# Kernel tuning notes

Measured on AMD Instinct MI355X. Metric: run time of the kernel, lower is better.

## Reference

```python
import jax, jax.numpy as jnp
from jax import lax
import numpy as np

B, T, DIN, DMID, DOUT = 8, 512, 512, 512, 128
KER = (0.15, 0.7, 0.15)  # 3-tap Gaussian blur, midnum fixed at 0.7 (deterministic stand-in for random.uniform(0.55,0.9))


def setup_inputs() -> dict:
    key = jax.random.key(0)
    ks = jax.random.split(key, 14)
    def lin(k, fi, fo):
        s = (6.0 / (fi + fo)) ** 0.5  # xavier-uniform
        return jax.random.uniform(k, (fi, fo), jnp.float32, -s, s)
    def convw(k, co, ci, kh, kw):
        s = (6.0 / (ci * kh * kw + co * kh * kw)) ** 0.5
        return jax.random.uniform(k, (co, ci, kh, kw), jnp.float32, -s, s)
    return {
        "seq": jax.random.normal(ks[0], (B, T, DIN), jnp.float32),
        "len_seq": jax.random.randint(ks[1], (B,), 256, T + 1, jnp.int32),
        "W1": lin(ks[2], DIN, DMID), "b1": jnp.zeros((DMID,), jnp.float32),
        "W2": lin(ks[3], DMID, DMID), "b2": jnp.zeros((DMID,), jnp.float32),
        "W3": lin(ks[4], DMID, DOUT), "b3": jnp.zeros((DOUT,), jnp.float32),
        "c1w": convw(ks[5], 30, 2, 5, 5), "c1b": jnp.zeros((30,), jnp.float32),
        "c2w": convw(ks[6], 30, 30, 5, 5), "c2b": jnp.zeros((30,), jnp.float32),
        "c3w": convw(ks[7], 1, 30, 3, 3), "c3b": jnp.zeros((1,), jnp.float32),
    }


def _mlp(x, W1, b1, W2, b2, W3, b3):
    # SequenceInception: linear-relu-linear-relu-linear, then L2 normalize with nan/inf -> 0
    h = jax.nn.relu(x @ W1 + b1)
    h = jax.nn.relu(h @ W2 + b2)
    o = h @ W3 + b3
    n = jnp.linalg.norm(o, axis=-1, keepdims=True)
    return jnp.nan_to_num(o / n, nan=0.0, posinf=0.0, neginf=0.0)


def _conv(x, w, b, pad):
    y = lax.conv_general_dilated(x, w, (1, 1), ((pad, pad), (pad, pad)),
                                 dimension_numbers=("NCHW", "OIHW", "NCHW"))
    return y + b[None, :, None, None]


def _blur(seq, len_seq):
    # BlurGenerationPair (Tc>4, 3-tap kernel, stride 1 branch), fully batched.
    k0, k1, k2 = KER
    blur = k0 * seq[:, :-2] + k1 * seq[:, 1:-1] + k2 * seq[:, 2:]  # [B, T-2, D]
    blur = jnp.pad(blur, ((0, 0), (0, 2), (0, 0)))
    t = jnp.arange(T)
    out_len = len_seq - 2
    out_mask = (t[None, :] < out_len[:, None]).astype(seq.dtype)      # [B, T]
    avged_seq = blur * out_mask[:, :, None]
    R = jnp.where(t[None] < len_seq[:, None], (t + 1.0) / len_seq[:, None].astype(jnp.float32), 0.0)
    avged_R = jnp.where(t[None] < out_len[:, None], (t + 1.0) / out_len[:, None].astype(jnp.float32), 0.0)
    # SeqtoBlur[b, i+o, i] = ker[o] for column i < out_len[b]
    base = k0 * jnp.eye(T) + k1 * jnp.eye(T, k=-1) + k2 * jnp.eye(T, k=-2)  # [T(row), T(col)]
    SeqtoBlur = base[None, :, :] * out_mask[:, None, :]
    sg = lax.stop_gradient
    return sg(SeqtoBlur), sg(avged_seq), sg(R), sg(avged_R), out_len


def reference(seq, len_seq, W1, b1, W2, b2, W3, b3, c1w, c1b, c2w, c2b, c3w, c3b):
    SeqtoBlur, avged_seq, R, avged_R, avged_len = _blur(seq, len_seq)
    emb_q = _mlp(seq, W1, b1, W2, b2, W3, b3)        # [B, T, DOUT]
    emb_k = _mlp(avged_seq, W1, b1, W2, b2, W3, b3)  # [B, T, DOUT]
    # OPA, batched over B (original asserts batch==1 and loops; same math per sample)
    sq = jnp.sum(emb_q * emb_q, -1)
    sk = jnp.sum(emb_k * emb_k, -1)
    g = jnp.einsum("bqd,bkd->bqk", emb_q, emb_k)
    D = jnp.sqrt(jnp.clip(sq[:, :, None] + sk[:, None, :] - 2.0 * g, 1e-12))  # cdist p=2
    P = jnp.abs(R[:, :, None] - avged_R[:, None, :])                           # 1-D cdist
    A = jnp.stack([D, P], axis=1)                    # [B, 2, T, T]
    A = jax.nn.relu(_conv(A, c1w, c1b, 2))
    A = jax.nn.relu(_conv(A, c2w, c2b, 2))
    A = _conv(A, c3w, c3b, 1)[:, 0] + D              # [B, T, T]
    S = jax.nn.softmax(-A, axis=2)
    At = S / jnp.sum(jnp.abs(S), axis=(1, 2), keepdims=True)  # L1 normalize over T*T
    dis = jnp.sum(D * At, axis=(1, 2))               # [B]
    return S, dis, SeqtoBlur, avged_len
```

## Files before the change

kernel.cpp:

```cpp
#include <hip/hip_runtime.h>
#include <hip/hip_bf16.h>

static constexpr size_t CHW = (size_t)512*512*32;

static constexpr size_t S_OFF    = 0;
static constexpr size_t DIS_OFF  = (size_t)8*512*512;
static constexpr size_t S2B_OFF  = DIS_OFF + 8;
static constexpr size_t ALEN_OFF = S2B_OFF + (size_t)8*512*512;

typedef __attribute__((ext_vector_type(8))) short bf16x8;
typedef __attribute__((ext_vector_type(4))) float f32x4;

__device__ __forceinline__ unsigned short rne_bf16(float x) {
  unsigned u = __builtin_bit_cast(unsigned, x);
  return (unsigned short)((u + 0x7FFFu + ((u >> 16) & 1u)) >> 16);
}
__device__ __forceinline__ unsigned pack_bf16x2(float lo, float hi) {
  return (unsigned)rne_bf16(lo) | ((unsigned)rne_bf16(hi) << 16);
}
__device__ __forceinline__ float bf2f(short s) {
  return __builtin_bit_cast(float, ((unsigned)(unsigned short)s) << 16);
}
__device__ __forceinline__ int chlog(int p) { return (p & 1) ? 16 + (p >> 1) : (p >> 1); }

__global__ __launch_bounds__(128) void megaprep(
    const float* __restrict__ seq, const int* __restrict__ len,
    const float* __restrict__ W1, const float* __restrict__ W2, const float* __restrict__ W3,
    const float* __restrict__ c1w, const float* __restrict__ c2w, const float* __restrict__ c3w,
    unsigned short* __restrict__ QKb,
    unsigned short* __restrict__ W1T, unsigned short* __restrict__ W2T,
    unsigned short* __restrict__ W3T,
    unsigned short* __restrict__ WB1m, unsigned char* __restrict__ WB2f,
    float* __restrict__ WT3, float* __restrict__ zpage,
    float* __restrict__ R, float* __restrict__ AR, float* __restrict__ alenOut,
    float* __restrict__ s2b) {
  int bid = blockIdx.x, tid = threadIdx.x;
  if (bid < 8192) {
    int t = bid & 511, b = (bid >> 9) & 7, mode = bid >> 12;
    size_t base = ((size_t)b*512 + t)*512 + tid*4;
    float v[4] = {0.f, 0.f, 0.f, 0.f};
    if (mode == 0) {
      float4 a = *(const float4*)&seq[base];
      v[0]=a.x; v[1]=a.y; v[2]=a.z; v[3]=a.w;
    } else {
      int OL = len[b] - 2;
      if (t < OL) {
        float4 a = *(const float4*)&seq[base];
        float4 c = *(const float4*)&seq[base + 512];
        float4 d = *(const float4*)&seq[base + 1024];
        v[0] = 0.15f*a.x + 0.7f*c.x + 0.15f*d.x;
        v[1] = 0.15f*a.y + 0.7f*c.y + 0.15f*d.y;
        v[2] = 0.15f*a.z + 0.7f*c.z + 0.15f*d.z;
        v[3] = 0.15f*a.w + 0.7f*c.w + 0.15f*d.w;
      }
    }
    ushort4 h;
    h.x = rne_bf16(v[0]); h.y = rne_bf16(v[1]);
    h.z = rne_bf16(v[2]); h.w = rne_bf16(v[3]);
    *(ushort4*)&QKb[((size_t)(mode*4096 + b*512 + t))*512 + tid*4] = h;
    return;
  }
  if (bid < 12288) {
    int r = bid - 8192;
    int i = r & 511, b = r >> 9;
    int OL = len[b] - 2;
    int j0 = tid*4;
    float vals[4];
#pragma unroll
    for (int e = 0; e < 4; ++e) {
      int j = j0 + e;
      float x = 0.f;
      if (j < OL) {
        if (j == i)        x = 0.15f;
        else if (j == i-1) x = 0.7f;
        else if (j == i-2) x = 0.15f;
      }
      vals[e] = x;
    }
    *(float4*)&s2b[((size_t)b*512 + i)*512 + j0] =
        make_float4(vals[0],vals[1],vals[2],vals[3]);
    return;
  }
  if (bid < 12320) {
    int r = bid - 12288;
    int b = r >> 2, t = (r & 3)*128 + tid;
    int L = len[b], OL = L - 2;
    R[b*512+t]  = (t < L)  ? (t+1.f)/(float)L  : 0.f;
    AR[b*512+t] = (t < OL) ? (t+1.f)/(float)OL : 0.f;
    if (t == 0) alenOut[b] = (float)OL;
    return;
  }
  if (bid < 13472) {
    int n = bid - 12320;
    const float* W; unsigned short* WT; int col, N;
    if (n < 512)       { W = W1; WT = W1T; col = n;        N = 512; }
    else if (n < 1024) { W = W2; WT = W2T; col = n - 512;  N = 512; }
    else               { W = W3; WT = W3T; col = n - 1024; N = 128; }
    for (int k = tid; k < 512; k += 128)
      WT[(size_t)col*512 + k] = rne_bf16(W[(size_t)k*N + col]);
    return;
  }
  if (tid < 64) zpage[tid] = 0.f;
  for (int i = tid; i < 7168; i += 128) {
    int ts = i >> 8, r = i & 255, oc = r >> 3, ch = r & 7;
    float v = 0.f;
    if (ts < 25 && oc < 30 && ch < 2) v = c1w[oc*50 + ch*25 + ts];
    WB1m[i] = rne_bf16(v);
  }
  for (int i = tid; i < 12800; i += 128) {
    int tap = i >> 9, r = i & 511, oc = r >> 4, jj = r & 15;
    float v0 = (oc < 30 && jj < 30)      ? c2w[(size_t)(oc*30 + jj)*25 + tap]      : 0.f;
    float v1 = (oc < 30 && 16 + jj < 30) ? c2w[(size_t)(oc*30 + 16 + jj)*25 + tap] : 0.f;
    int pk = __builtin_amdgcn_cvt_pk_fp8_f32(v0, v1, 0, false);
    ((unsigned short*)WB2f)[(tap*32 + oc)*16 + jj] = (unsigned short)pk;
  }
  for (int i = tid; i < 288; i += 128) {
    int tap = i >> 5, icp = i & 31;
    int icl = chlog(icp);
    WT3[i] = (icl < 30) ? c3w[icl*9 + tap] : 0.f;
  }
}

template<int OUTMODE>
__global__ __launch_bounds__(256) void gemm_bf(
    const unsigned short* __restrict__ A, const unsigned short* __restrict__ B,
    const float* __restrict__ bias, float* __restrict__ Cf,
    unsigned short* __restrict__ Cb, int M, int N, int K) {
  __shared__ short sA[128*40], sB[64*40];
  int tid = threadIdx.x, l = tid & 63, w = tid >> 6;
  int wm = w >> 1, wn = w & 1;
  int rowBase = blockIdx.y * 128, colBase = blockIdx.x * 64;
  int lr = l & 15, lc = l >> 4;
  f32x4 acc[4][2] = {};
  for (int k0 = 0; k0 < K; k0 += 32) {
    int idx = tid;
#pragma unroll
    for (int it = 0; it < 2; ++it, idx += 256) {
      int row = idx >> 2, c = (idx & 3) * 8;
      *(bf16x8*)&sA[row*40 + c] = *(const bf16x8*)&A[(size_t)(rowBase + row)*K + k0 + c];
    }
    {
      int row = tid >> 2, c = (tid & 3) * 8;
      if (row < 64)
        *(bf16x8*)&sB[row*40 + c] = *(const bf16x8*)&B[(size_t)(colBase + row)*K + k0 + c];
    }
    __syncthreads();
    bf16x8 a[4], b[2];
#pragma unroll
    for (int m = 0; m < 4; ++m)
      a[m] = *(const bf16x8*)&sA[(wm*64 + m*16 + lr)*40 + lc*8];
#pragma unroll
    for (int n = 0; n < 2; ++n)
      b[n] = *(const bf16x8*)&sB[(wn*32 + n*16 + lr)*40 + lc*8];
#pragma unroll
    for (int m = 0; m < 4; ++m)
#pragma unroll
      for (int n = 0; n < 2; ++n)
        acc[m][n] = __builtin_amdgcn_mfma_f32_16x16x32_bf16(a[m], b[n], acc[m][n], 0, 0, 0);
    __syncthreads();
  }
#pragma unroll
  for (int m = 0; m < 4; ++m) {
    int row = rowBase + wm*64 + m*16 + lc*4;
#pragma unroll
    for (int n = 0; n < 2; ++n) {
      int col = colBase + wn*32 + n*16 + lr;
      float bv = bias[col];
#pragma unroll
      for (int j = 0; j < 4; ++j) {
        float v = acc[m][n][j] + bv;
        size_t o = (size_t)(row + j) * N + col;
        if (OUTMODE == 1) Cb[o] = rne_bf16(fmaxf(v, 0.f));
        else              Cf[o] = v;
      }
    }
  }
}

__global__ __launch_bounds__(64) void norm_kernel(const float* __restrict__ EMB,
    unsigned short* __restrict__ Eb, float* __restrict__ sqn) {
  int row = blockIdx.x, tid = threadIdx.x;
  size_t base = (size_t)row * 128;
  float v0 = EMB[base + tid], v1 = EMB[base + tid + 64];
  float ss = v0*v0 + v1*v1;
#pragma unroll
  for (int off = 32; off; off >>= 1) ss += __shfl_xor(ss, off);
  float n = sqrtf(ss);
  float inv = (n > 0.f) ? 1.f/n : 0.f;
  Eb[base + tid]      = rne_bf16(v0 * inv);
  Eb[base + tid + 64] = rne_bf16(v1 * inv);
  if (tid == 0) sqn[row] = ss * inv * inv;
}

__global__ __launch_bounds__(256) void dmat_mfma(const unsigned short* __restrict__ Eb,
    const float* __restrict__ sqn, float* __restrict__ Dm) {
  __shared__ short sQ[64*40], sK[64*40];
  int tid = threadIdx.x, l = tid & 63, w = tid >> 6;
  int wm = w >> 1, wn = w & 1;
  int kBase = blockIdx.x * 64, qBase = blockIdx.y * 64, b = blockIdx.z;
  const unsigned short* Q  = Eb + (size_t)b*512*128;
  const unsigned short* Kp = Eb + (size_t)(4096 + b*512)*128;
  int lr = l & 15, lc = l >> 4;
  f32x4 acc[2][2] = {};
  for (int k0 = 0; k0 < 128; k0 += 32) {
    int row = tid >> 2, c = (tid & 3) * 8;
    *(bf16x8*)&sQ[row*40 + c] = *(const bf16x8*)&Q[(size_t)(qBase + row)*128 + k0 + c];
    *(bf16x8*)&sK[row*40 + c] = *(const bf16x8*)&Kp[(size_t)(kBase + row)*128 + k0 + c];
    __syncthreads();
    bf16x8 q[2], k[2];
#pragma unroll
    for (int m = 0; m < 2; ++m) q[m] = *(const bf16x8*)&sQ[(wm*32 + m*16 + lr)*40 + lc*8];
#pragma unroll
    for (int n = 0; n < 2; ++n) k[n] = *(const bf16x8*)&sK[(wn*32 + n*16 + lr)*40 + lc*8];
#pragma unroll
    for (int m = 0; m < 2; ++m)
#pragma unroll
      for (int n = 0; n < 2; ++n)
        acc[m][n] = __builtin_amdgcn_mfma_f32_16x16x32_bf16(q[m], k[n], acc[m][n], 0, 0, 0);
    __syncthreads();
  }
#pragma unroll
  for (int m = 0; m < 2; ++m) {
#pragma unroll
    for (int n = 0; n < 2; ++n) {
      int k = kBase + wn*32 + n*16 + lr;
      float skv = sqn[4096 + b*512 + k];
#pragma unroll
      for (int j = 0; j < 4; ++j) {
        int q = qBase + wm*32 + m*16 + lc*4 + j;
        float sqv = sqn[b*512 + q];
        float d2 = fmaxf(sqv + skv - 2.f*acc[m][n][j], 1e-12f);
        Dm[((size_t)b*512 + q)*512 + k] = sqrtf(d2);
      }
    }
  }
}

__global__ __launch_bounds__(256) void conv1_mfma(const float* __restrict__ Dm,
    const float* __restrict__ R, const float* __restrict__ AR,
    unsigned char* __restrict__ cbout, const unsigned short* __restrict__ WB1m,
    const float* __restrict__ bias, int b0) {
  __shared__ short tile[36*20*8];
  int tid = threadIdx.x, l = tid & 63, w = tid >> 6;
  int x0 = blockIdx.x * 16, y0 = blockIdx.y * 32, slot = blockIdx.z;
  int b = b0 + slot;
  for (int i = tid; i < 720; i += 256) {
    int r = i / 20, c = i - r*20;
    int gy = y0 - 2 + r, gx = x0 - 2 + c;
    float dv = 0.f, pv = 0.f;
    if ((unsigned)gy < 512u && (unsigned)gx < 512u) {
      dv = Dm[((size_t)b*512 + gy)*512 + gx];
      pv = fabsf(R[b*512 + gy] - AR[b*512 + gx]);
    }
    bf16x8 v = {};
    v[0] = (short)rne_bf16(dv);
    v[1] = (short)rne_bf16(pv);
    *(bf16x8*)&tile[i*8] = v;
  }
  __syncthreads();
  int lr = l & 15, lc = l >> 4;
  f32x4 acc[8][2] = {};
  int wy = w * 8;
  bf16x8 pb0 = *(const bf16x8*)&WB1m[(size_t)lc*256 + lr*8];
  bf16x8 pb1 = *(const bf16x8*)&WB1m[(size_t)lc*256 + (16 + lr)*8];
  __builtin_amdgcn_s_setprio(1);
#pragma unroll
  for (int m = 0; m < 7; ++m) {
    int t = m*4 + lc;
    int ky = t / 5, kx = t - ky*5;
    bool valid = (t < 25);
    bf16x8 b0 = pb0, b1 = pb1;
    if (m < 6) {
      int tn = (m+1)*4 + lc;
      pb0 = *(const bf16x8*)&WB1m[(size_t)tn*256 + lr*8];
      pb1 = *(const bf16x8*)&WB1m[(size_t)tn*256 + (16 + lr)*8];
    }
#pragma unroll
    for (int g = 0; g < 8; ++g) {
      bf16x8 a = {};
      if (valid) a = *(const bf16x8*)&tile[((wy + g + ky)*20 + lr + kx)*8];
      acc[g][0] = __builtin_amdgcn_mfma_f32_16x16x32_bf16(a, b0, acc[g][0], 0, 0, 0);
      acc[g][1] = __builtin_amdgcn_mfma_f32_16x16x32_bf16(a, b1, acc[g][1], 0, 0, 0);
    }
  }
  __builtin_amdgcn_s_setprio(0);
  unsigned char* outp = cbout + (size_t)slot * CHW;
  float bv0 = bias[lr];
  float bv1 = (16 + lr < 30) ? bias[16 + lr] : 0.f;
#pragma unroll
  for (int g = 0; g < 8; ++g) {
    int y = y0 + wy + g;
#pragma unroll
    for (int j = 0; j < 4; ++j) {
      int px = x0 + lc*4 + j;
      size_t ob = ((size_t)y*512 + px)*32;
      int pk = __builtin_amdgcn_cvt_pk_fp8_f32(
          fmaxf(acc[g][0][j] + bv0, 0.f), fmaxf(acc[g][1][j] + bv1, 0.f), 0, false);
      *(unsigned short*)&outp[ob + 2*lr] = (unsigned short)pk;
    }
  }
}

__global__ __launch_bounds__(256, 4) void conv2_mfma(const unsigned char* __restrict__ cbin,
    unsigned short* __restrict__ cbout, const unsigned char* __restrict__ WB2f,
    const float* __restrict__ bias, const float* __restrict__ zpage) {
  __shared__ char tile[36*20*32];
  int tid = threadIdx.x, l = tid & 63, w = tid >> 6;
  int x0 = blockIdx.x * 16, y0 = blockIdx.y * 32, slot = blockIdx.z;
  const unsigned char* in = cbin + (size_t)slot * CHW;
  for (int idx = tid; idx < 1440; idx += 256) {
    int cs = idx & 1, px = idx >> 1;
    int r = px / 20, cc = px - r*20;
    int c16 = cs ^ ((cc >> 1) & 1);
    int gy = y0 - 2 + r, gx = x0 - 2 + cc;
    const void* src = ((unsigned)gy < 512u && (unsigned)gx < 512u)
        ? (const void*)&in[((size_t)gy*512 + gx)*32 + c16*16]
        : (const void*)zpage;
    __builtin_amdgcn_global_load_lds(
        (const __attribute__((address_space(1))) void*)src,
        (__attribute__((address_space(3))) void*)&tile[(size_t)idx*16], 16, 0, 0);
  }
  __syncthreads();
  int lr = l & 15, lc = l >> 4;
  f32x4 acc[8][2] = {};
  int wy = w * 8;
  long long pb0[2], pb1[2];
  {
    pb0[0] = *(const long long*)&WB2f[(size_t)(0*32 + lr)*32 + lc*8];
    pb1[0] = *(const long long*)&WB2f[(size_t)(0*32 + 16 + lr)*32 + lc*8];
    pb0[1] = *(const long long*)&WB2f[(size_t)(5*32 + lr)*32 + lc*8];
    pb1[1] = *(const long long*)&WB2f[(size_t)(5*32 + 16 + lr)*32 + lc*8];
  }
  __builtin_amdgcn_s_setprio(1);
#pragma unroll
  for (int kx = 0; kx < 5; ++kx) {
    int x = lr + kx;
    int s = (((lc >> 1) ^ ((x >> 1) & 1)) << 1) | (lc & 1);
    long long a[12];
#pragma unroll
    for (int r = 0; r < 12; ++r)
      a[r] = *(const long long*)&tile[((wy + r)*20 + x)*32 + s*8];
#pragma unroll
    for (int ky = 0; ky < 5; ++ky) {
      int i = kx*5 + ky;
      int sq = i & 1;
      long long b0 = pb0[sq], b1 = pb1[sq];
      int in2 = i + 2;
      if (in2 < 25) {
        int nkx = in2 / 5, nky = in2 - nkx*5;
        int ntap = nky*5 + nkx;
        pb0[sq] = *(const long long*)&WB2f[(size_t)(ntap*32 + lr)*32 + lc*8];
        pb1[sq] = *(const long long*)&WB2f[(size_t)(ntap*32 + 16 + lr)*32 + lc*8];
      }
#pragma unroll
      for (int g = 0; g < 8; ++g) {
        acc[g][0] = __builtin_amdgcn_mfma_f32_16x16x32_fp8_fp8(a[g+ky], b0, acc[g][0], 0, 0, 0);
        acc[g][1] = __builtin_amdgcn_mfma_f32_16x16x32_fp8_fp8(a[g+ky], b1, acc[g][1], 0, 0, 0);
      }
    }
  }
  __builtin_amdgcn_s_setprio(0);
  unsigned short* outp = cbout + (size_t)slot * CHW;
  float bv0 = (lr < 30) ? bias[lr] : 0.f;
  float bv1 = 0.f;
  if (16 + lr < 30) bv1 = bias[16 + lr];
#pragma unroll
  for (int g = 0; g < 8; ++g) {
    int y = y0 + wy + g;
#pragma unroll
    for (int j = 0; j < 4; ++j) {
      int px = x0 + lc*4 + j;
      size_t ob = ((size_t)y*512 + px)*32;
      *(unsigned*)&outp[ob + 2*lr] =
          pack_bf16x2(fmaxf(acc[g][0][j] + bv0, 0.f), fmaxf(acc[g][1][j] + bv1, 0.f));
    }
  }
}

__global__ __launch_bounds__(256) void conv3_nhwc(const unsigned short* __restrict__ cbin,
    const float* __restrict__ Dm, const float* __restrict__ WT3,
    const float* __restrict__ b3c, float* __restrict__ A3, int b0) {
  int slot = blockIdx.z, b = b0 + slot;
  int tid = threadIdx.x, tx = tid & 15, ty = tid >> 4;
  int x0 = blockIdx.x * 16, y0 = blockIdx.y * 16;
  __shared__ short tile[18*18*40];
  const unsigned short* in = cbin + (size_t)slot * CHW;
  for (int idx = tid; idx < 1296; idx += 256) {
    int c = (idx & 3) * 8, px = idx >> 2;
    int r = px / 18, cc = px - r*18;
    int gy = y0 - 1 + r, gx = x0 - 1 + cc;
    bf16x8 v = {};
    if ((unsigned)gy < 512u && (unsigned)gx < 512u)
      v = *(const bf16x8*)&in[((size_t)gy*512 + gx)*32 + c];
    *(bf16x8*)&tile[(r*18 + cc)*40 + c] = v;
  }
  __syncthreads();
  float acc = 0.f;
#pragma unroll
  for (int ky = 0; ky < 3; ++ky) {
#pragma unroll
    for (int kx = 0; kx < 3; ++kx) {
      const float* wp = &WT3[(ky*3 + kx)*32];
      int base = ((ty+ky)*18 + tx+kx)*40;
#pragma unroll
      for (int c = 0; c < 4; ++c) {
        bf16x8 v = *(const bf16x8*)&tile[base + c*8];
#pragma unroll
        for (int j = 0; j < 8; ++j)
          acc = fmaf(bf2f(v[j]), wp[c*8 + j], acc);
      }
    }
  }
  size_t o = ((size_t)b*512 + y0 + ty)*512 + x0 + tx;
  A3[o] = acc + b3c[0] + Dm[o];
}

__global__ __launch_bounds__(256) void softmax_kernel(const float* __restrict__ A3,
    const float* __restrict__ Dm, float* __restrict__ S,
    float* __restrict__ rowDS, float* __restrict__ rowSS) {
  __shared__ float sred[4];
  __shared__ float sred2[4], sred3[4];
  int q = blockIdx.x, b = blockIdx.y, tid = threadIdx.x;
  size_t base = ((size_t)b*512 + q)*512;
  float x0 = -A3[base + tid], x1 = -A3[base + tid + 256];
  float m = fmaxf(x0, x1);
#pragma unroll
  for (int off = 32; off; off >>= 1) m = fmaxf(m, __shfl_xor(m, off));
  if ((tid & 63) == 0) sred[tid >> 6] = m;
  __syncthreads();
  m = fmaxf(fmaxf(sred[0], sred[1]), fmaxf(sred[2], sred[3]));
  __syncthreads();
  float p0 = expf(x0 - m), p1 = expf(x1 - m);
  float s = p0 + p1;
#pragma unroll
  for (int off = 32; off; off >>= 1) s += __shfl_xor(s, off);
  if ((tid & 63) == 0) sred[tid >> 6] = s;
  __syncthreads();
  s = sred[0] + sred[1] + sred[2] + sred[3];
  float inv = 1.f / s;
  float s0 = p0 * inv, s1 = p1 * inv;
  S[base + tid] = s0;
  S[base + tid + 256] = s1;
  float ds = s0*Dm[base + tid] + s1*Dm[base + tid + 256];
  float ssum = s0 + s1;
#pragma unroll
  for (int off = 32; off; off >>= 1) { ds += __shfl_xor(ds, off); ssum += __shfl_xor(ssum, off); }
  if ((tid & 63) == 0) { sred2[tid>>6] = ds; sred3[tid>>6] = ssum; }
  __syncthreads();
  if (tid == 0) {
    rowDS[b*512+q] = sred2[0]+sred2[1]+sred2[2]+sred2[3];
    rowSS[b*512+q] = sred3[0]+sred3[1]+sred3[2]+sred3[3];
  }
}

__global__ __launch_bounds__(512) void dis_kernel(const float* __restrict__ rowDS,
    const float* __restrict__ rowSS, float* __restrict__ disOut) {
  __shared__ float sd[8], se[8];
  int b = blockIdx.x, tid = threadIdx.x;
  float ds = rowDS[b*512 + tid];
  float ss = rowSS[b*512 + tid];
#pragma unroll
  for (int off = 32; off; off >>= 1) { ds += __shfl_xor(ds, off); ss += __shfl_xor(ss, off); }
  if ((tid & 63) == 0) { sd[tid>>6] = ds; se[tid>>6] = ss; }
  __syncthreads();
  if (tid == 0) {
    float a = 0.f, c = 0.f;
    for (int i = 0; i < 8; ++i) { a += sd[i]; c += se[i]; }
    disOut[b] = a / c;
  }
}

extern "C" void kernel_launch(void* const* d_in, const int* in_sizes, int n_in,
                              void* d_out, int out_size, void* d_ws, size_t ws_size,
                              hipStream_t stream) {
  const float* seq = (const float*)d_in[0];
  const int*   len = (const int*)d_in[1];
  const float* W1  = (const float*)d_in[2];  const float* b1 = (const float*)d_in[3];
  const float* W2  = (const float*)d_in[4];  const float* b2 = (const float*)d_in[5];
  const float* W3  = (const float*)d_in[6];  const float* b3 = (const float*)d_in[7];
  const float* c1w = (const float*)d_in[8];  const float* c1b = (const float*)d_in[9];
  const float* c2w = (const float*)d_in[10]; const float* c2b = (const float*)d_in[11];
  const float* c3w = (const float*)d_in[12]; const float* c3b = (const float*)d_in[13];
  float* out = (float*)d_out;
  char*  ws  = (char*)d_ws;

  size_t off = 0;
  auto alloc = [&](size_t bytes) { size_t o = off; off = (off + bytes + 255) & ~(size_t)255; return o; };
  const size_t MK2 = (size_t)8192*512*2;
  unsigned short* QKb = (unsigned short*)(ws + alloc(MK2));
  unsigned short* H1  = (unsigned short*)(ws + alloc(MK2));
  unsigned short* H2  = (unsigned short*)(ws + alloc(MK2));
  float* EMB = (float*)(ws + alloc((size_t)8192*128*4));
  unsigned short* EMBb = (unsigned short*)(ws + alloc((size_t)8192*128*2));
  float* SQN = (float*)(ws + alloc(8192*4));
  float* Rb  = (float*)(ws + alloc(4096*4));
  float* ARb = (float*)(ws + alloc(4096*4));
  float* Db  = (float*)(ws + alloc((size_t)8*512*512*4));
  float* A3  = (float*)(ws + alloc((size_t)8*512*512*4));
  float* RDS = (float*)(ws + alloc(4096*4));
  float* RSS = (float*)(ws + alloc(4096*4));
  unsigned short* W1T = (unsigned short*)(ws + alloc((size_t)512*512*2));
  unsigned short* W2T = (unsigned short*)(ws + alloc((size_t)512*512*2));
  unsigned short* W3T = (unsigned short*)(ws + alloc((size_t)128*512*2));
  unsigned short* WB1m = (unsigned short*)(ws + alloc(7168*2));
  unsigned char* WB2f = (unsigned char*)(ws + alloc(25600));
  float* WT3 = (float*)(ws + alloc(288*4));
  float* ZPG = (float*)(ws + alloc(256));
  size_t fixed = off;

  int nb = 1;
  const size_t CB1B = CHW;
  const size_t CB2B = CHW * 2;
  if      (fixed + 8*(CB1B + CB2B) <= ws_size) nb = 8;
  else if (fixed + 4*(CB1B + CB2B) <= ws_size) nb = 4;
  else if (fixed + 2*(CB1B + CB2B) <= ws_size) nb = 2;
  unsigned char*  CB1 = (unsigned char*)(ws + alloc((size_t)nb*CB1B));
  unsigned short* CB2 = (unsigned short*)(ws + alloc((size_t)nb*CB2B));

  megaprep<<<13473, 128, 0, stream>>>(seq, len, W1, W2, W3, c1w, c2w, c3w,
      QKb, W1T, W2T, W3T, WB1m, WB2f, WT3, ZPG, Rb, ARb, out + ALEN_OFF, out + S2B_OFF);

  gemm_bf<1><<<dim3(8, 64), 256, 0, stream>>>(QKb, W1T, b1, nullptr, H1, 8192, 512, 512);
  gemm_bf<1><<<dim3(8, 64), 256, 0, stream>>>(H1,  W2T, b2, nullptr, H2, 8192, 512, 512);
  gemm_bf<0><<<dim3(2, 64), 256, 0, stream>>>(H2,  W3T, b3, EMB, nullptr, 8192, 128, 512);
  norm_kernel<<<8192, 64, 0, stream>>>(EMB, EMBb, SQN);
  dmat_mfma<<<dim3(8,8,8), 256, 0, stream>>>(EMBb, SQN, Db);

  for (int bb = 0; bb < 8; bb += nb) {
    conv1_mfma<<<dim3(32,16,nb), 256, 0, stream>>>(Db, Rb, ARb, CB1, WB1m, c1b, bb);
    conv2_mfma<<<dim3(32,16,nb), 256, 0, stream>>>(CB1, CB2, WB2f, c2b, ZPG);
    conv3_nhwc<<<dim3(32,32,nb), 256, 0, stream>>>(CB2, Db, WT3, c3b, A3, bb);
  }

  softmax_kernel<<<dim3(512,8), 256, 0, stream>>>(A3, Db, out + S_OFF, RDS, RSS);
  dis_kernel<<<8, 512, 0, stream>>>(RDS, RSS, out + DIS_OFF);
}
```

Measured before the change: 269.5 us.

## Use 16x16x128 scaled FP8 MFMA for conv2, packing four taps per K

Conv2 now uses the MI355X scaled MFMA with K=128 in place of the 16x16x32 FP8 MFMA. Each lane group handles a different tap, so four 5x5 taps are reduced per instruction, padded to 28 taps with zero weights. The LDS tile swizzle and the weight buffer layout are changed to match the wider 32-byte fragments, and the register double-buffered weight prefetch is dropped. This cuts the MFMA instruction count by about 4x, at the cost of some padded work and more per-lane LDS traffic.

Result: no change. 271.9 us (+0.9%).

```diff
diff --git a/kernel.cpp b/kernel.cpp
--- a/kernel.cpp
+++ b/kernel.cpp
@@ -10,6 +10,8 @@
 
 typedef __attribute__((ext_vector_type(8))) short bf16x8;
 typedef __attribute__((ext_vector_type(4))) float f32x4;
+typedef __attribute__((ext_vector_type(4))) int   i32x4;
+typedef __attribute__((ext_vector_type(8))) int   i32x8;
 
 __device__ __forceinline__ unsigned short rne_bf16(float x) {
   unsigned u = __builtin_bit_cast(unsigned, x);
@@ -107,10 +109,13 @@
     if (ts < 25 && oc < 30 && ch < 2) v = c1w[oc*50 + ch*25 + ts];
     WB1m[i] = rne_bf16(v);
   }
-  for (int i = tid; i < 12800; i += 128) {
+  for (int i = tid; i < 14336; i += 128) {
     int tap = i >> 9, r = i & 511, oc = r >> 4, jj = r & 15;
-    float v0 = (oc < 30 && jj < 30)      ? c2w[(size_t)(oc*30 + jj)*25 + tap]      : 0.f;
-    float v1 = (oc < 30 && 16 + jj < 30) ? c2w[(size_t)(oc*30 + 16 + jj)*25 + tap] : 0.f;
+    float v0 = 0.f, v1 = 0.f;
+    if (tap < 25 && oc < 30) {
+      if (jj < 30)      v0 = c2w[(size_t)(oc*30 + jj)*25 + tap];
+      if (16 + jj < 30) v1 = c2w[(size_t)(oc*30 + 16 + jj)*25 + tap];
+    }
     int pk = __builtin_amdgcn_cvt_pk_fp8_f32(v0, v1, 0, false);
     ((unsigned short*)WB2f)[(tap*32 + oc)*16 + jj] = (unsigned short)pk;
   }
@@ -311,7 +316,7 @@
   for (int idx = tid; idx < 1440; idx += 256) {
     int cs = idx & 1, px = idx >> 1;
     int r = px / 20, cc = px - r*20;
-    int c16 = cs ^ ((cc >> 1) & 1);
+    int c16 = cs ^ ((px >> 2) & 1);
     int gy = y0 - 2 + r, gx = x0 - 2 + cc;
     const void* src = ((unsigned)gy < 512u && (unsigned)gx < 512u)
         ? (const void*)&in[((size_t)gy*512 + gx)*32 + c16*16]
@@ -324,39 +329,30 @@
   int lr = l & 15, lc = l >> 4;
   f32x4 acc[8][2] = {};
   int wy = w * 8;
-  long long pb0[2], pb1[2];
-  {
-    pb0[0] = *(const long long*)&WB2f[(size_t)(0*32 + lr)*32 + lc*8];
-    pb1[0] = *(const long long*)&WB2f[(size_t)(0*32 + 16 + lr)*32 + lc*8];
-    pb0[1] = *(const long long*)&WB2f[(size_t)(5*32 + lr)*32 + lc*8];
-    pb1[1] = *(const long long*)&WB2f[(size_t)(5*32 + 16 + lr)*32 + lc*8];
-  }
   __builtin_amdgcn_s_setprio(1);
 #pragma unroll
-  for (int kx = 0; kx < 5; ++kx) {
-    int x = lr + kx;
-    int s = (((lc >> 1) ^ ((x >> 1) & 1)) << 1) | (lc & 1);
-    long long a[12];
-#pragma unroll
-    for (int r = 0; r < 12; ++r)
-      a[r] = *(const long long*)&tile[((wy + r)*20 + x)*32 + s*8];
-#pragma unroll
-    for (int ky = 0; ky < 5; ++ky) {
-      int i = kx*5 + ky;
-      int sq = i & 1;
-      long long b0 = pb0[sq], b1 = pb1[sq];
-      int in2 = i + 2;
-      if (in2 < 25) {
-        int nkx = in2 / 5, nky = in2 - nkx*5;
-        int ntap = nky*5 + nkx;
-        pb0[sq] = *(const long long*)&WB2f[(size_t)(ntap*32 + lr)*32 + lc*8];
-        pb1[sq] = *(const long long*)&WB2f[(size_t)(ntap*32 + 16 + lr)*32 + lc*8];
-      }
-#pragma unroll
-      for (int g = 0; g < 8; ++g) {
-        acc[g][0] = __builtin_amdgcn_mfma_f32_16x16x32_fp8_fp8(a[g+ky], b0, acc[g][0], 0, 0, 0);
-        acc[g][1] = __builtin_amdgcn_mfma_f32_16x16x32_fp8_fp8(a[g+ky], b1, acc[g][1], 0, 0, 0);
-      }
+  for (int m = 0; m < 7; ++m) {
+    int t = m*4 + lc;
+    int tc = (t < 25) ? t : 24;
+    int ky = tc / 5, kx = tc - ky*5;
+    const unsigned char* wp0 = &WB2f[(size_t)(t*32 + lr)*32];
+    const unsigned char* wp1 = &WB2f[(size_t)(t*32 + 16 + lr)*32];
+    i32x4 w0a = *(const i32x4*)wp0, w0b = *(const i32x4*)(wp0 + 16);
+    i32x4 w1a = *(const i32x4*)wp1, w1b = *(const i32x4*)(wp1 + 16);
+    i32x8 b0f = {w0a[0], w0a[1], w0a[2], w0a[3], w0b[0], w0b[1], w0b[2], w0b[3]};
+    i32x8 b1f = {w1a[0], w1a[1], w1a[2], w1a[3], w1b[0], w1b[1], w1b[2], w1b[3]};
+#pragma unroll
+    for (int g = 0; g < 8; ++g) {
+      int p = (wy + g + ky)*20 + lr + kx;
+      int sw = (p >> 2) & 1;
+      const char* base = &tile[p*32];
+      i32x4 alo = *(const i32x4*)(base + sw*16);
+      i32x4 ahi = *(const i32x4*)(base + 16 - sw*16);
+      i32x8 af = {alo[0], alo[1], alo[2], alo[3], ahi[0], ahi[1], ahi[2], ahi[3]};
+      acc[g][0] = __builtin_amdgcn_mfma_scale_f32_16x16x128_f8f6f4(
+          af, b0f, acc[g][0], 0, 0, 0, 127u, 0, 127u);
+      acc[g][1] = __builtin_amdgcn_mfma_scale_f32_16x16x128_f8f6f4(
+          af, b1f, acc[g][1], 0, 0, 0, 127u, 0, 127u);
     }
   }
   __builtin_amdgcn_s_setprio(0);
@@ -503,7 +499,7 @@
   unsigned short* W2T = (unsigned short*)(ws + alloc((size_t)512*512*2));
   unsigned short* W3T = (unsigned short*)(ws + alloc((size_t)128*512*2));
   unsigned short* WB1m = (unsigned short*)(ws + alloc(7168*2));
-  unsigned char* WB2f = (unsigned char*)(ws + alloc(25600));
+  unsigned char* WB2f = (unsigned char*)(ws + alloc(28672));
   float* WT3 = (float*)(ws + alloc(288*4));
   float* ZPG = (float*)(ws + alloc(256));
   size_t fixed = off;
```
